# Performance work log

Hardware: AMD Instinct MI355X
Metric: run time of the kernel (lower is better)

The kernel has to match this reference:

```python
import jax, jax.numpy as jnp
import numpy as np

HID, HEADS, HD = 512, 8, 64  # hid_dim, n_heads, head_dim
NEG = -1e10


def setup_inputs() -> dict:
    key = jax.random.key(0)
    ks = jax.random.split(key, 12)
    B, S = 4, 2048
    inp = {
        'query': jax.random.normal(ks[0], (B, S, HID), jnp.float32),
        'key': jax.random.normal(ks[1], (B, S, HID), jnp.float32),
        'value': jax.random.normal(ks[2], (B, S, HID), jnp.float32),
        'mask': jnp.ones((B, 1, 1, S), jnp.int32),
    }
    sc = 1.0 / np.sqrt(HID)
    for i, n in enumerate(['Wq', 'Wk', 'Wv', 'Wo']):
        inp[n] = jax.random.uniform(ks[3 + i], (HID, HID), jnp.float32, -sc, sc)
    for i, n in enumerate(['bq', 'bk', 'bv', 'bo']):
        inp[n] = jax.random.uniform(ks[7 + i], (HID,), jnp.float32, -sc, sc)
    return inp


def reference(query, key, value, mask, Wq, Wk, Wv, Wo, bq, bk, bv, bo):
    B = query.shape[0]

    def proj(x, W, b):
        # torch Linear: x @ W.T + b; then split heads -> [B, H, S, HD]
        y = jnp.einsum('bsd,ed->bse', x, W) + b
        return y.reshape(B, -1, HEADS, HD).transpose(0, 2, 1, 3)

    Q = proj(query, Wq, bq)
    K = proj(key, Wk, bk)
    V = proj(value, Wv, bv)
    scale = jnp.sqrt(jnp.float32(HD))
    E = jnp.einsum('bhqd,bhkd->bhqk', Q, K) / scale  # [B,H,Sq,Sk]
    E = jnp.where(mask == 0, NEG, E)
    A = jax.nn.softmax(E, axis=-1)  # dropout p=0 -> identity
    out = jnp.einsum('bhqk,bhkd->bhqd', A, V)
    out = out.transpose(0, 2, 1, 3).reshape(B, -1, HID)
    return jnp.einsum('bsd,ed->bse', out, Wo) + bo
```

## Files before the change

kernel.cpp:

```cpp
#include <hip/hip_runtime.h>
#include <hip/hip_bf16.h>


typedef __bf16 v8bf __attribute__((ext_vector_type(8)));
typedef __bf16 v4bf __attribute__((ext_vector_type(4)));
typedef float  v4f  __attribute__((ext_vector_type(4)));

#define MFMA16(a, b, c) __builtin_amdgcn_mfma_f32_16x16x32_bf16((a), (b), (c), 0, 0, 0)

__device__ __forceinline__ void gl16(const __bf16* g, __bf16* l) {
    __builtin_amdgcn_global_load_lds(
        (const __attribute__((address_space(1))) void*)g,
        (__attribute__((address_space(3))) void*)l, 16, 0, 0);
}

__device__ inline v8bf cvt8(const float* __restrict__ p) {
    const v4f f0 = *(const v4f*)p;
    const v4f f1 = *(const v4f*)(p + 4);
    v8bf r;
    r[0] = (__bf16)f0[0]; r[1] = (__bf16)f0[1]; r[2] = (__bf16)f0[2]; r[3] = (__bf16)f0[3];
    r[4] = (__bf16)f1[0]; r[5] = (__bf16)f1[1]; r[6] = (__bf16)f1[2]; r[7] = (__bf16)f1[3];
    return r;
}

__global__ __launch_bounds__(256) void cvt_w(
    const float* __restrict__ Wq, const float* __restrict__ Wk,
    const float* __restrict__ Wv, const float* __restrict__ Wo,
    __bf16* __restrict__ out)
{
    const int idx = (blockIdx.x * 256 + threadIdx.x) * 4;
    const int w = idx >> 18, off = idx & 262143;
    const float* src = (w == 0) ? Wq : (w == 1) ? Wk : (w == 2) ? Wv : Wo;
    const v4f x = *(const v4f*)(src + off);
    v4bf y;
    y[0] = (__bf16)x[0]; y[1] = (__bf16)x[1]; y[2] = (__bf16)x[2]; y[3] = (__bf16)x[3];
    *(v4bf*)(out + idx) = y;
}

__global__ __launch_bounds__(256) void cvt_x(
    const float* __restrict__ xq, const float* __restrict__ xk,
    const float* __restrict__ xv, __bf16* __restrict__ out)
{
    const int idx = (blockIdx.x * 256 + threadIdx.x) * 8;
    const int w = idx >> 22, off = idx & 4194303;
    const float* src = (w == 0) ? xq : (w == 1) ? xk : xv;
    *(v8bf*)(out + idx) = cvt8(src + off);
}

__global__ __launch_bounds__(256) void qkv_gemm(
    const __bf16* __restrict__ xb, const __bf16* __restrict__ Wb,
    const float* __restrict__ bq, const float* __restrict__ bk, const float* __restrict__ bv,
    __bf16* __restrict__ Qo, __bf16* __restrict__ Ko, __bf16* __restrict__ VTo)
{
    const int z = blockIdx.z;
    const __bf16* x    = xb + (size_t)z * 4194304;
    const __bf16* W    = Wb + (size_t)z * 262144;
    const float*  bias = (z == 0) ? bq : (z == 1) ? bk : bv;

    const int tid = threadIdx.x, wave = tid >> 6, lane = tid & 63;
    const int quad = lane >> 4, r = lane & 15;
    const int wm = wave >> 1, wn = wave & 1;
    const int row0 = blockIdx.x * 128, col0 = blockIdx.y * 128;

    __shared__ __align__(16) __bf16 As[8192];
    __shared__ __align__(16) __bf16 Bs[8192];

    const __bf16* aG[4];
    const __bf16* bG[4];
    __bf16* aL[4];
    __bf16* bL[4];
    for (int j = 0; j < 4; j++) {
        const int s = wave * 4 + j;
        aG[j] = x + (size_t)(row0 + (s >> 1) * 16 + r) * 512 + (s & 1) * 32 + quad * 8;
        bG[j] = W + (size_t)(col0 + (s >> 1) * 16 + r) * 512 + (s & 1) * 32 + quad * 8;
        aL[j] = &As[s * 512];
        bL[j] = &Bs[s * 512];
    }

    v4f acc[4][4] = {};

    for (int ki = 0; ki < 8; ki++) {
        const int kk = ki * 64;
        __syncthreads();
        for (int j = 0; j < 4; j++) {
            gl16(aG[j] + kk, aL[j]);
            gl16(bG[j] + kk, bL[j]);
        }
        __syncthreads();
        for (int kc = 0; kc < 2; kc++) {
            v8bf a[4], b[4];
            for (int i = 0; i < 4; i++)
                a[i] = ((const v8bf*)As)[((wm * 4 + i) * 2 + kc) * 64 + lane];
            for (int i = 0; i < 4; i++)
                b[i] = ((const v8bf*)Bs)[((wn * 4 + i) * 2 + kc) * 64 + lane];
            for (int mi = 0; mi < 4; mi++)
                for (int ni = 0; ni < 4; ni++)
                    acc[mi][ni] = MFMA16(a[mi], b[ni], acc[mi][ni]);
        }
    }

    for (int ni = 0; ni < 4; ni++) {
        const int n = col0 + wn * 64 + ni * 16 + r;
        const float bv_ = bias[n];
        const int hh = n >> 6, hd = n & 63;
        for (int mi = 0; mi < 4; mi++) {
            const int mbase = row0 + wm * 64 + mi * 16 + quad * 4;
            const int bb = mbase >> 11, s0 = mbase & 2047;
            if (z == 2) {
                v4bf pk;
                for (int i = 0; i < 4; i++)
                    pk[i] = (__bf16)(acc[mi][ni][i] + bv_);
                *(v4bf*)&VTo[((size_t)((bb * 8 + hh) * 64 + hd)) * 2048 + s0] = pk;
            } else {
                __bf16* dst = (z == 0) ? Qo : Ko;
                for (int i = 0; i < 4; i++)
                    dst[((size_t)((bb * 8 + hh) * 2048 + s0 + i)) * 64 + hd] =
                        (__bf16)(acc[mi][ni][i] + bv_);
            }
        }
    }
}

__global__ __launch_bounds__(256, 2) void attn(
    const __bf16* __restrict__ Q, const __bf16* __restrict__ K,
    const __bf16* __restrict__ VT, const int* __restrict__ mask,
    __bf16* __restrict__ AO)
{
    const int id = blockIdx.y * 16 + blockIdx.x;
    const int x8 = id & 7, j = (id >> 3) & 3, qb = id >> 5;
    const int bh = x8 * 4 + j;
    const int b = bh >> 3, h = bh & 7;
    const int tid = threadIdx.x, wave = tid >> 6, lane = tid & 63;
    const int quad = lane >> 4, r = lane & 15;
    const int q0 = qb * 128 + wave * 32;

    const __bf16* Qb = Q  + (size_t)bh * 2048 * 64;
    const __bf16* Kb = K  + (size_t)bh * 2048 * 64;
    const __bf16* Vb = VT + (size_t)bh * 64 * 2048;
    const int*    mb = mask + (size_t)b * 2048;

    __shared__ __align__(16) __bf16 Kls[4096];
    __shared__ __align__(16) __bf16 Vls[4096];
    __shared__ __align__(16) float  biasF[2048];
    __shared__ __align__(16) __bf16 Pls[4][2][16][72];

    for (int i = tid; i < 2048; i += 256)
        biasF[i] = (mb[i] != 0) ? 0.f : -1.0e10f;

    const int e1 = tid, e2 = tid + 256;
    int seg, l, t_, h_, rr, qd;
    seg = e1 >> 6; l = e1 & 63; t_ = seg >> 1; h_ = seg & 1; rr = l & 15; qd = l >> 4;
    const __bf16* kg1 = Kb + (size_t)(16 * t_ + rr) * 64   + h_ * 32 + qd * 8;
    const __bf16* vg1 = Vb + (size_t)(16 * t_ + rr) * 2048 + h_ * 32 + qd * 8;
    seg = e2 >> 6; l = e2 & 63; t_ = seg >> 1; h_ = seg & 1; rr = l & 15; qd = l >> 4;
    const __bf16* kg2 = Kb + (size_t)(16 * t_ + rr) * 64   + h_ * 32 + qd * 8;
    const __bf16* vg2 = Vb + (size_t)(16 * t_ + rr) * 2048 + h_ * 32 + qd * 8;

    v8bf qf[2][2];
    for (int g = 0; g < 2; g++) {
        qf[g][0] = *(const v8bf*)(Qb + (size_t)(q0 + g * 16 + r) * 64 +      quad * 8);
        qf[g][1] = *(const v8bf*)(Qb + (size_t)(q0 + g * 16 + r) * 64 + 32 + quad * 8);
    }

    v8bf ones;
    for (int i = 0; i < 8; i++) ones[i] = (__bf16)1.0f;

    v4f o[2][4] = {};
    v4f osum[2] = {};

    const float SC = 0.18033688f;

    v8bf ks1 = *(const v8bf*)kg1, ks2 = *(const v8bf*)kg2;
    v8bf vs1 = *(const v8bf*)vg1, vs2 = *(const v8bf*)vg2;

    for (int t = 0; t < 32; t++) {
        __syncthreads();
        ((v8bf*)Kls)[e1] = ks1; ((v8bf*)Kls)[e2] = ks2;
        ((v8bf*)Vls)[e1] = vs1; ((v8bf*)Vls)[e2] = vs2;
        __syncthreads();
        if (t < 31) {
            const int k0n = (t + 1) * 64;
            ks1 = *(const v8bf*)(kg1 + (size_t)k0n * 64);
            ks2 = *(const v8bf*)(kg2 + (size_t)k0n * 64);
            vs1 = *(const v8bf*)(vg1 + k0n);
            vs2 = *(const v8bf*)(vg2 + k0n);
        }
        const int k0 = t * 64;

        v4f sa[2][4] = {};
        for (int tt = 0; tt < 4; tt++) {
            const v8bf kf0 = ((const v8bf*)Kls)[(tt * 2 + 0) * 64 + lane];
            const v8bf kf1 = ((const v8bf*)Kls)[(tt * 2 + 1) * 64 + lane];
            sa[0][tt] = MFMA16(kf0, qf[0][0], sa[0][tt]);
            sa[0][tt] = MFMA16(kf1, qf[0][1], sa[0][tt]);
            sa[1][tt] = MFMA16(kf0, qf[1][0], sa[1][tt]);
            sa[1][tt] = MFMA16(kf1, qf[1][1], sa[1][tt]);
        }

        for (int tt = 0; tt < 4; tt++) {
            const v4f bl = *(const v4f*)&biasF[k0 + tt * 16 + quad * 4];
            for (int g = 0; g < 2; g++) {
                v4bf pk;
                for (int i = 0; i < 4; i++) {
                    const float p = __builtin_amdgcn_exp2f(fmaf(sa[g][tt][i], SC, bl[i]));
                    pk[i] = (__bf16)p;
                }
                *(v4bf*)&Pls[wave][g][r][tt * 16 + quad * 4] = pk;
            }
        }
        asm volatile("s_waitcnt lgkmcnt(0)" ::: "memory");
        v8bf pa[2][2];
        for (int g = 0; g < 2; g++) {
            pa[g][0] = *(const v8bf*)&Pls[wave][g][r][     quad * 8];
            pa[g][1] = *(const v8bf*)&Pls[wave][g][r][32 + quad * 8];
        }

        osum[0] = MFMA16(pa[0][0], ones, osum[0]);
        osum[0] = MFMA16(pa[0][1], ones, osum[0]);
        osum[1] = MFMA16(pa[1][0], ones, osum[1]);
        osum[1] = MFMA16(pa[1][1], ones, osum[1]);

        for (int t2 = 0; t2 < 4; t2++) {
            const v8bf vf0 = ((const v8bf*)Vls)[(t2 * 2 + 0) * 64 + lane];
            const v8bf vf1 = ((const v8bf*)Vls)[(t2 * 2 + 1) * 64 + lane];
            o[0][t2] = MFMA16(pa[0][0], vf0, o[0][t2]);
            o[0][t2] = MFMA16(pa[0][1], vf1, o[0][t2]);
            o[1][t2] = MFMA16(pa[1][0], vf0, o[1][t2]);
            o[1][t2] = MFMA16(pa[1][1], vf1, o[1][t2]);
        }
    }

    for (int g = 0; g < 2; g++) {
        float inv[4];
        for (int i = 0; i < 4; i++) inv[i] = 1.0f / osum[g][i];
        for (int t2 = 0; t2 < 4; t2++) {
            const int hd = t2 * 16 + r;
            for (int i = 0; i < 4; i++) {
                const int s = q0 + g * 16 + quad * 4 + i;
                AO[((size_t)b * 2048 + s) * 512 + h * 64 + hd] =
                    (__bf16)(o[g][t2][i] * inv[i]);
            }
        }
    }
}

__global__ __launch_bounds__(256) void out_gemm(
    const __bf16* __restrict__ Ai, const __bf16* __restrict__ W,
    const float* __restrict__ bias, float* __restrict__ y)
{
    const int tid = threadIdx.x, wave = tid >> 6, lane = tid & 63;
    const int quad = lane >> 4, r = lane & 15;
    const int wm = wave >> 1, wn = wave & 1;
    const int row0 = blockIdx.x * 64, col0 = blockIdx.y * 128;

    __shared__ __align__(16) __bf16 As[4096];
    __shared__ __align__(16) __bf16 Bs[8192];

    const __bf16* aG[2];
    const __bf16* bG[4];
    __bf16* aL[2];
    __bf16* bL[4];
    for (int j = 0; j < 2; j++) {
        const int s = wave * 2 + j;
        aG[j] = Ai + (size_t)(row0 + (s >> 1) * 16 + r) * 512 + (s & 1) * 32 + quad * 8;
        aL[j] = &As[s * 512];
    }
    for (int j = 0; j < 4; j++) {
        const int s = wave * 4 + j;
        bG[j] = W + (size_t)(col0 + (s >> 1) * 16 + r) * 512 + (s & 1) * 32 + quad * 8;
        bL[j] = &Bs[s * 512];
    }

    v4f acc[2][4] = {};

    for (int ki = 0; ki < 8; ki++) {
        const int kk = ki * 64;
        __syncthreads();
        gl16(aG[0] + kk, aL[0]);
        gl16(aG[1] + kk, aL[1]);
        for (int j = 0; j < 4; j++)
            gl16(bG[j] + kk, bL[j]);
        __syncthreads();
        for (int kc = 0; kc < 2; kc++) {
            v8bf a[2], b[4];
            for (int i = 0; i < 2; i++)
                a[i] = ((const v8bf*)As)[((wm * 2 + i) * 2 + kc) * 64 + lane];
            for (int i = 0; i < 4; i++)
                b[i] = ((const v8bf*)Bs)[((wn * 4 + i) * 2 + kc) * 64 + lane];
            for (int mi = 0; mi < 2; mi++)
                for (int ni = 0; ni < 4; ni++)
                    acc[mi][ni] = MFMA16(a[mi], b[ni], acc[mi][ni]);
        }
    }

    for (int ni = 0; ni < 4; ni++) {
        const int n = col0 + wn * 64 + ni * 16 + r;
        const float bv_ = bias[n];
        for (int mi = 0; mi < 2; mi++) {
            const int mbase = row0 + wm * 32 + mi * 16 + quad * 4;
            for (int i = 0; i < 4; i++)
                y[(size_t)(mbase + i) * 512 + n] = acc[mi][ni][i] + bv_;
        }
    }
}

extern "C" void kernel_launch(void* const* d_in, const int* in_sizes, int n_in,
                              void* d_out, int out_size, void* d_ws, size_t ws_size,
                              hipStream_t stream)
{
    const float* q    = (const float*)d_in[0];
    const float* k    = (const float*)d_in[1];
    const float* v    = (const float*)d_in[2];
    const int*   mask = (const int*)d_in[3];
    const float* Wq   = (const float*)d_in[4];
    const float* Wk   = (const float*)d_in[5];
    const float* Wv   = (const float*)d_in[6];
    const float* Wo   = (const float*)d_in[7];
    const float* bq   = (const float*)d_in[8];
    const float* bk   = (const float*)d_in[9];
    const float* bv   = (const float*)d_in[10];
    const float* bo   = (const float*)d_in[11];

    __bf16* ws  = (__bf16*)d_ws;
    __bf16* Qw  = ws;
    __bf16* Kw  = ws + 4194304;
    __bf16* VTw = ws + 8388608;
    __bf16* AOw = ws + 12582912;
    __bf16* Wb  = ws + 16777216;
    __bf16* xbw = ws + 17825792;

    cvt_w<<<dim3(1024), 256, 0, stream>>>(Wq, Wk, Wv, Wo, Wb);
    cvt_x<<<dim3(6144), 256, 0, stream>>>(q, k, v, xbw);
    qkv_gemm<<<dim3(64, 4, 3), 256, 0, stream>>>(xbw, Wb, bq, bk, bv, Qw, Kw, VTw);
    attn<<<dim3(16, 32), 256, 0, stream>>>(Qw, Kw, VTw, mask, AOw);
    out_gemm<<<dim3(128, 4), 256, 0, stream>>>(AOw, Wb + 786432, bo, (float*)d_out);
}
```

Before: 206.9 us.

## Double-buffer LDS in GEMMs and attention, merge conversion kernels, repack P

Both projection GEMMs now use two LDS buffers with a BK=32 loop, so async global-to-LDS loads of the next slice overlap the MFMAs on the current one and each iteration needs one barrier instead of two. The attention kernel double-buffers K/V in LDS, writing the next tile after the current compute so each step has a single barrier. It also stores P in a fragment-native layout so it can be read back with one contiguous 16-byte load per lane. The two fp32-to-bf16 conversion kernels are merged into one launch to save launch overhead. In exchange LDS use grows (attention roughly doubles K/V storage), which could lower occupancy, and the GEMMs now run 16 shorter iterations.

```diff
diff --git a/kernel.cpp b/kernel.cpp
--- a/kernel.cpp
+++ b/kernel.cpp
@@ -23,28 +23,28 @@
     return r;
 }
 
-__global__ __launch_bounds__(256) void cvt_w(
+__global__ __launch_bounds__(256) void cvt_all(
     const float* __restrict__ Wq, const float* __restrict__ Wk,
     const float* __restrict__ Wv, const float* __restrict__ Wo,
-    __bf16* __restrict__ out)
-{
-    const int idx = (blockIdx.x * 256 + threadIdx.x) * 4;
-    const int w = idx >> 18, off = idx & 262143;
-    const float* src = (w == 0) ? Wq : (w == 1) ? Wk : (w == 2) ? Wv : Wo;
-    const v4f x = *(const v4f*)(src + off);
-    v4bf y;
-    y[0] = (__bf16)x[0]; y[1] = (__bf16)x[1]; y[2] = (__bf16)x[2]; y[3] = (__bf16)x[3];
-    *(v4bf*)(out + idx) = y;
-}
-
-__global__ __launch_bounds__(256) void cvt_x(
     const float* __restrict__ xq, const float* __restrict__ xk,
-    const float* __restrict__ xv, __bf16* __restrict__ out)
-{
-    const int idx = (blockIdx.x * 256 + threadIdx.x) * 8;
-    const int w = idx >> 22, off = idx & 4194303;
-    const float* src = (w == 0) ? xq : (w == 1) ? xk : xv;
-    *(v8bf*)(out + idx) = cvt8(src + off);
+    const float* __restrict__ xv,
+    __bf16* __restrict__ Wb, __bf16* __restrict__ xb)
+{
+    const int bid = blockIdx.x;
+    if (bid < 1024) {
+        const int idx = (bid * 256 + threadIdx.x) * 4;
+        const int w = idx >> 18, off = idx & 262143;
+        const float* src = (w == 0) ? Wq : (w == 1) ? Wk : (w == 2) ? Wv : Wo;
+        const v4f x = *(const v4f*)(src + off);
+        v4bf y;
+        y[0] = (__bf16)x[0]; y[1] = (__bf16)x[1]; y[2] = (__bf16)x[2]; y[3] = (__bf16)x[3];
+        *(v4bf*)(Wb + idx) = y;
+    } else {
+        const int idx = ((bid - 1024) * 256 + threadIdx.x) * 8;
+        const int w = idx >> 22, off = idx & 4194303;
+        const float* src = (w == 0) ? xq : (w == 1) ? xk : xv;
+        *(v8bf*)(xb + idx) = cvt8(src + off);
+    }
 }
 
 __global__ __launch_bounds__(256) void qkv_gemm(
@@ -62,41 +62,45 @@
     const int wm = wave >> 1, wn = wave & 1;
     const int row0 = blockIdx.x * 128, col0 = blockIdx.y * 128;
 
-    __shared__ __align__(16) __bf16 As[8192];
-    __shared__ __align__(16) __bf16 Bs[8192];
-
-    const __bf16* aG[4];
-    const __bf16* bG[4];
-    __bf16* aL[4];
-    __bf16* bL[4];
-    for (int j = 0; j < 4; j++) {
-        const int s = wave * 4 + j;
-        aG[j] = x + (size_t)(row0 + (s >> 1) * 16 + r) * 512 + (s & 1) * 32 + quad * 8;
-        bG[j] = W + (size_t)(col0 + (s >> 1) * 16 + r) * 512 + (s & 1) * 32 + quad * 8;
-        aL[j] = &As[s * 512];
-        bL[j] = &Bs[s * 512];
+    __shared__ __align__(16) __bf16 As[2][4096];
+    __shared__ __align__(16) __bf16 Bs[2][4096];
+
+    const __bf16* aG[2];
+    const __bf16* bG[2];
+    int aOff[2];
+    for (int j = 0; j < 2; j++) {
+        const int s = wave * 2 + j;
+        aG[j] = x + (size_t)(row0 + s * 16 + r) * 512 + quad * 8;
+        bG[j] = W + (size_t)(col0 + s * 16 + r) * 512 + quad * 8;
+        aOff[j] = s * 512;
     }
 
     v4f acc[4][4] = {};
 
-    for (int ki = 0; ki < 8; ki++) {
-        const int kk = ki * 64;
+    for (int j = 0; j < 2; j++) {
+        gl16(aG[j], &As[0][aOff[j]]);
+        gl16(bG[j], &Bs[0][aOff[j]]);
+    }
+    __syncthreads();
+
+    for (int t = 0; t < 16; t++) {
+        const int cur = t & 1;
+        if (t < 15) {
+            const int kk = (t + 1) * 32;
+            for (int j = 0; j < 2; j++) {
+                gl16(aG[j] + kk, &As[cur ^ 1][aOff[j]]);
+                gl16(bG[j] + kk, &Bs[cur ^ 1][aOff[j]]);
+            }
+        }
+        v8bf a[4], b[4];
+        for (int i = 0; i < 4; i++)
+            a[i] = ((const v8bf*)As[cur])[(wm * 4 + i) * 64 + lane];
+        for (int i = 0; i < 4; i++)
+            b[i] = ((const v8bf*)Bs[cur])[(wn * 4 + i) * 64 + lane];
+        for (int mi = 0; mi < 4; mi++)
+            for (int ni = 0; ni < 4; ni++)
+                acc[mi][ni] = MFMA16(a[mi], b[ni], acc[mi][ni]);
         __syncthreads();
-        for (int j = 0; j < 4; j++) {
-            gl16(aG[j] + kk, aL[j]);
-            gl16(bG[j] + kk, bL[j]);
-        }
-        __syncthreads();
-        for (int kc = 0; kc < 2; kc++) {
-            v8bf a[4], b[4];
-            for (int i = 0; i < 4; i++)
-                a[i] = ((const v8bf*)As)[((wm * 4 + i) * 2 + kc) * 64 + lane];
-            for (int i = 0; i < 4; i++)
-                b[i] = ((const v8bf*)Bs)[((wn * 4 + i) * 2 + kc) * 64 + lane];
-            for (int mi = 0; mi < 4; mi++)
-                for (int ni = 0; ni < 4; ni++)
-                    acc[mi][ni] = MFMA16(a[mi], b[ni], acc[mi][ni]);
-        }
     }
 
     for (int ni = 0; ni < 4; ni++) {
@@ -139,10 +143,10 @@
     const __bf16* Vb = VT + (size_t)bh * 64 * 2048;
     const int*    mb = mask + (size_t)b * 2048;
 
-    __shared__ __align__(16) __bf16 Kls[4096];
-    __shared__ __align__(16) __bf16 Vls[4096];
+    __shared__ __align__(16) __bf16 Kls[2][4096];
+    __shared__ __align__(16) __bf16 Vls[2][4096];
     __shared__ __align__(16) float  biasF[2048];
-    __shared__ __align__(16) __bf16 Pls[4][2][16][72];
+    __shared__ __align__(16) __bf16 PF[4][4][64][8];
 
     for (int i = tid; i < 2048; i += 256)
         biasF[i] = (mb[i] != 0) ? 0.f : -1.0e10f;
@@ -170,27 +174,28 @@
 
     const float SC = 0.18033688f;
 
+    const int entE = (quad >> 1) * 16 + r;
+    const int entO = entE + 32;
+    const int eoff = (quad & 1) * 4;
+
     v8bf ks1 = *(const v8bf*)kg1, ks2 = *(const v8bf*)kg2;
     v8bf vs1 = *(const v8bf*)vg1, vs2 = *(const v8bf*)vg2;
-
+    ((v8bf*)Kls[0])[e1] = ks1; ((v8bf*)Kls[0])[e2] = ks2;
+    ((v8bf*)Vls[0])[e1] = vs1; ((v8bf*)Vls[0])[e2] = vs2;
+    ks1 = *(const v8bf*)(kg1 + (size_t)64 * 64);
+    ks2 = *(const v8bf*)(kg2 + (size_t)64 * 64);
+    vs1 = *(const v8bf*)(vg1 + 64);
+    vs2 = *(const v8bf*)(vg2 + 64);
+    __syncthreads();
+
+    int cur = 0;
     for (int t = 0; t < 32; t++) {
-        __syncthreads();
-        ((v8bf*)Kls)[e1] = ks1; ((v8bf*)Kls)[e2] = ks2;
-        ((v8bf*)Vls)[e1] = vs1; ((v8bf*)Vls)[e2] = vs2;
-        __syncthreads();
-        if (t < 31) {
-            const int k0n = (t + 1) * 64;
-            ks1 = *(const v8bf*)(kg1 + (size_t)k0n * 64);
-            ks2 = *(const v8bf*)(kg2 + (size_t)k0n * 64);
-            vs1 = *(const v8bf*)(vg1 + k0n);
-            vs2 = *(const v8bf*)(vg2 + k0n);
-        }
         const int k0 = t * 64;
 
         v4f sa[2][4] = {};
         for (int tt = 0; tt < 4; tt++) {
-            const v8bf kf0 = ((const v8bf*)Kls)[(tt * 2 + 0) * 64 + lane];
-            const v8bf kf1 = ((const v8bf*)Kls)[(tt * 2 + 1) * 64 + lane];
+            const v8bf kf0 = ((const v8bf*)Kls[cur])[(tt * 2 + 0) * 64 + lane];
+            const v8bf kf1 = ((const v8bf*)Kls[cur])[(tt * 2 + 1) * 64 + lane];
             sa[0][tt] = MFMA16(kf0, qf[0][0], sa[0][tt]);
             sa[0][tt] = MFMA16(kf1, qf[0][1], sa[0][tt]);
             sa[1][tt] = MFMA16(kf0, qf[1][0], sa[1][tt]);
@@ -199,20 +204,22 @@
 
         for (int tt = 0; tt < 4; tt++) {
             const v4f bl = *(const v4f*)&biasF[k0 + tt * 16 + quad * 4];
+            const int ent = (tt & 1) ? entO : entE;
+            const int pl = tt >> 1;
             for (int g = 0; g < 2; g++) {
                 v4bf pk;
                 for (int i = 0; i < 4; i++) {
                     const float p = __builtin_amdgcn_exp2f(fmaf(sa[g][tt][i], SC, bl[i]));
                     pk[i] = (__bf16)p;
                 }
-                *(v4bf*)&Pls[wave][g][r][tt * 16 + quad * 4] = pk;
+                *(v4bf*)&PF[wave][g * 2 + pl][ent][eoff] = pk;
             }
         }
         asm volatile("s_waitcnt lgkmcnt(0)" ::: "memory");
         v8bf pa[2][2];
         for (int g = 0; g < 2; g++) {
-            pa[g][0] = *(const v8bf*)&Pls[wave][g][r][     quad * 8];
-            pa[g][1] = *(const v8bf*)&Pls[wave][g][r][32 + quad * 8];
+            pa[g][0] = *(const v8bf*)&PF[wave][g * 2 + 0][lane][0];
+            pa[g][1] = *(const v8bf*)&PF[wave][g * 2 + 1][lane][0];
         }
 
         osum[0] = MFMA16(pa[0][0], ones, osum[0]);
@@ -221,13 +228,27 @@
         osum[1] = MFMA16(pa[1][1], ones, osum[1]);
 
         for (int t2 = 0; t2 < 4; t2++) {
-            const v8bf vf0 = ((const v8bf*)Vls)[(t2 * 2 + 0) * 64 + lane];
-            const v8bf vf1 = ((const v8bf*)Vls)[(t2 * 2 + 1) * 64 + lane];
+            const v8bf vf0 = ((const v8bf*)Vls[cur])[(t2 * 2 + 0) * 64 + lane];
+            const v8bf vf1 = ((const v8bf*)Vls[cur])[(t2 * 2 + 1) * 64 + lane];
             o[0][t2] = MFMA16(pa[0][0], vf0, o[0][t2]);
             o[0][t2] = MFMA16(pa[0][1], vf1, o[0][t2]);
             o[1][t2] = MFMA16(pa[1][0], vf0, o[1][t2]);
             o[1][t2] = MFMA16(pa[1][1], vf1, o[1][t2]);
         }
+
+        if (t < 31) {
+            ((v8bf*)Kls[cur ^ 1])[e1] = ks1; ((v8bf*)Kls[cur ^ 1])[e2] = ks2;
+            ((v8bf*)Vls[cur ^ 1])[e1] = vs1; ((v8bf*)Vls[cur ^ 1])[e2] = vs2;
+            if (t < 30) {
+                const int k0n = (t + 2) * 64;
+                ks1 = *(const v8bf*)(kg1 + (size_t)k0n * 64);
+                ks2 = *(const v8bf*)(kg2 + (size_t)k0n * 64);
+                vs1 = *(const v8bf*)(vg1 + k0n);
+                vs2 = *(const v8bf*)(vg2 + k0n);
+            }
+        }
+        __syncthreads();
+        cur ^= 1;
     }
 
     for (int g = 0; g < 2; g++) {
@@ -253,44 +274,43 @@
     const int wm = wave >> 1, wn = wave & 1;
     const int row0 = blockIdx.x * 64, col0 = blockIdx.y * 128;
 
-    __shared__ __align__(16) __bf16 As[4096];
-    __shared__ __align__(16) __bf16 Bs[8192];
-
-    const __bf16* aG[2];
-    const __bf16* bG[4];
-    __bf16* aL[2];
-    __bf16* bL[4];
+    __shared__ __align__(16) __bf16 As[2][2048];
+    __shared__ __align__(16) __bf16 Bs[2][4096];
+
+    const __bf16* aG = Ai + (size_t)(row0 + wave * 16 + r) * 512 + quad * 8;
+    const int aOff = wave * 512;
+    const __bf16* bG[2];
+    int bOff[2];
     for (int j = 0; j < 2; j++) {
         const int s = wave * 2 + j;
-        aG[j] = Ai + (size_t)(row0 + (s >> 1) * 16 + r) * 512 + (s & 1) * 32 + quad * 8;
-        aL[j] = &As[s * 512];
-    }
-    for (int j = 0; j < 4; j++) {
-        const int s = wave * 4 + j;
-        bG[j] = W + (size_t)(col0 + (s >> 1) * 16 + r) * 512 + (s & 1) * 32 + quad * 8;
-        bL[j] = &Bs[s * 512];
+        bG[j] = W + (size_t)(col0 + s * 16 + r) * 512 + quad * 8;
+        bOff[j] = s * 512;
     }
 
     v4f acc[2][4] = {};
 
-    for (int ki = 0; ki < 8; ki++) {
-        const int kk = ki * 64;
+    gl16(aG, &As[0][aOff]);
+    gl16(bG[0], &Bs[0][bOff[0]]);
+    gl16(bG[1], &Bs[0][bOff[1]]);
+    __syncthreads();
+
+    for (int t = 0; t < 16; t++) {
+        const int cur = t & 1;
+        if (t < 15) {
+            const int kk = (t + 1) * 32;
+            gl16(aG + kk, &As[cur ^ 1][aOff]);
+            gl16(bG[0] + kk, &Bs[cur ^ 1][bOff[0]]);
+            gl16(bG[1] + kk, &Bs[cur ^ 1][bOff[1]]);
+        }
+        v8bf a[2], b[4];
+        for (int i = 0; i < 2; i++)
+            a[i] = ((const v8bf*)As[cur])[(wm * 2 + i) * 64 + lane];
+        for (int i = 0; i < 4; i++)
+            b[i] = ((const v8bf*)Bs[cur])[(wn * 4 + i) * 64 + lane];
+        for (int mi = 0; mi < 2; mi++)
+            for (int ni = 0; ni < 4; ni++)
+                acc[mi][ni] = MFMA16(a[mi], b[ni], acc[mi][ni]);
         __syncthreads();
-        gl16(aG[0] + kk, aL[0]);
-        gl16(aG[1] + kk, aL[1]);
-        for (int j = 0; j < 4; j++)
-            gl16(bG[j] + kk, bL[j]);
-        __syncthreads();
-        for (int kc = 0; kc < 2; kc++) {
-            v8bf a[2], b[4];
-            for (int i = 0; i < 2; i++)
-                a[i] = ((const v8bf*)As)[((wm * 2 + i) * 2 + kc) * 64 + lane];
-            for (int i = 0; i < 4; i++)
-                b[i] = ((const v8bf*)Bs)[((wn * 4 + i) * 2 + kc) * 64 + lane];
-            for (int mi = 0; mi < 2; mi++)
-                for (int ni = 0; ni < 4; ni++)
-                    acc[mi][ni] = MFMA16(a[mi], b[ni], acc[mi][ni]);
-        }
     }
 
     for (int ni = 0; ni < 4; ni++) {
@@ -329,8 +349,7 @@
     __bf16* Wb  = ws + 16777216;
     __bf16* xbw = ws + 17825792;
 
-    cvt_w<<<dim3(1024), 256, 0, stream>>>(Wq, Wk, Wv, Wo, Wb);
-    cvt_x<<<dim3(6144), 256, 0, stream>>>(q, k, v, xbw);
+    cvt_all<<<dim3(7168), 256, 0, stream>>>(Wq, Wk, Wv, Wo, q, k, v, Wb, xbw);
     qkv_gemm<<<dim3(64, 4, 3), 256, 0, stream>>>(xbw, Wb, bq, bk, bv, Qw, Kw, VTw);
     attn<<<dim3(16, 32), 256, 0, stream>>>(Qw, Kw, VTw, mask, AOw);
     out_gemm<<<dim3(128, 4), 256, 0, stream>>>(AOw, Wb + 786432, bo, (float*)d_out);
```

Result: no change. 207.2 us (+0.2%).
